# Kernel optimization log

Hardware: AMD Instinct MI355X
Metric: run time of the kernel (lower is better)

## Reference

```python
import jax, jax.numpy as jnp
import numpy as np

D_MODEL = 1024
N_HEADS = 16
HEAD_DIM = D_MODEL // N_HEADS
SPARSITY = 0.5  # torch.rand(...) < sparsity_factor -> True means masked (disallowed)


def setup_inputs() -> dict:
    key = jax.random.key(0)
    ks = jax.random.split(key, 12)
    B, S, D = 2, 2048, D_MODEL
    query = jax.random.normal(ks[0], (B, S, D), dtype=jnp.float32)
    key_t = jax.random.normal(ks[1], (B, S, D), dtype=jnp.float32)
    value = jax.random.normal(ks[2], (B, S, D), dtype=jnp.float32)
    # per-forward random boolean mask, materialized deterministically here
    mask = jax.random.uniform(ks[3], (B, S, S)) < SPARSITY
    scale = 1.0 / np.sqrt(D)
    Wq = jax.random.uniform(ks[4], (D, D), jnp.float32, -scale, scale)
    Wk = jax.random.uniform(ks[5], (D, D), jnp.float32, -scale, scale)
    Wv = jax.random.uniform(ks[6], (D, D), jnp.float32, -scale, scale)
    Wo = jax.random.uniform(ks[7], (D, D), jnp.float32, -scale, scale)
    bq = jnp.zeros((D,), jnp.float32)
    bk = jnp.zeros((D,), jnp.float32)
    bv = jnp.zeros((D,), jnp.float32)
    bo = jnp.zeros((D,), jnp.float32)
    return {"query": query, "key": key_t, "value": value, "mask": mask,
            "Wq": Wq, "Wk": Wk, "Wv": Wv, "Wo": Wo,
            "bq": bq, "bk": bk, "bv": bv, "bo": bo}


def reference(query, key, value, mask, Wq, Wk, Wv, Wo, bq, bk, bv, bo):
    B, S, D = query.shape
    H, hd = N_HEADS, HEAD_DIM
    # in-projections (torch uses x @ W.T + b)
    q = (query @ Wq.T + bq).reshape(B, S, H, hd).transpose(0, 2, 1, 3)  # (B,H,S,hd)
    k = (key @ Wk.T + bk).reshape(B, S, H, hd).transpose(0, 2, 1, 3)
    v = (value @ Wv.T + bv).reshape(B, S, H, hd).transpose(0, 2, 1, 3)
    scores = jnp.einsum('bhqd,bhkd->bhqk', q, k) / jnp.sqrt(jnp.float32(hd))
    # bool mask: True = disallowed; broadcast over heads
    scores = jnp.where(mask[:, None, :, :], -jnp.inf, scores)
    attn = jax.nn.softmax(scores, axis=-1)  # dropout inactive at eval
    out = jnp.einsum('bhqk,bhkd->bhqd', attn, v)  # (B,H,S,hd)
    out = out.transpose(0, 2, 1, 3).reshape(B, S, D)
    return out @ Wo.T + bo
```

## Files before the change

### kernel.cpp

```cpp
#include <hip/hip_runtime.h>
#include <stdint.h>

#define MTOK   4096
#define DMODEL 1024
#define SEQ    2048
#define NH     16
#define HD     64
#define LDK    72
#define LDP    72
#define QSCL   0.18033688f
#define NWORDS (2 * SEQ * SEQ / 64)

typedef _Float16 h8  __attribute__((ext_vector_type(8)));
typedef _Float16 h4  __attribute__((ext_vector_type(4)));
typedef _Float16 h2  __attribute__((ext_vector_type(2)));
typedef __fp16   fp16x2 __attribute__((ext_vector_type(2)));
typedef float    f16v __attribute__((ext_vector_type(16)));
typedef float    f4  __attribute__((ext_vector_type(4)));

typedef __attribute__((address_space(1))) const unsigned int g_u32;
typedef __attribute__((address_space(3))) unsigned int       l_u32;

__device__ __forceinline__ void g2l16(const void* g, void* l) {
    __builtin_amdgcn_global_load_lds((g_u32*)(unsigned long long)g,
                                     (l_u32*)(unsigned int)(unsigned long long)l,
                                     16, 0, 0);
}

__device__ __forceinline__ h2 pkrtz(float a, float b) {
    fp16x2 r = __builtin_amdgcn_cvt_pkrtz(a, b);
    return __builtin_bit_cast(h2, r);
}

#if __has_builtin(__builtin_amdgcn_exp2f)
#define E2(x) __builtin_amdgcn_exp2f(x)
#else
#define E2(x) exp2f(x)
#endif

__global__ __launch_bounds__(256) void prep_kernel(
    const float* __restrict__ s0, const float* __restrict__ s1,
    const float* __restrict__ s2, const float* __restrict__ s3,
    const float* __restrict__ s4, const float* __restrict__ s5,
    const float* __restrict__ s6,
    _Float16* __restrict__ d0, _Float16* __restrict__ d1,
    _Float16* __restrict__ d2, _Float16* __restrict__ d3,
    _Float16* __restrict__ d4, _Float16* __restrict__ d5,
    _Float16* __restrict__ d6,
    const unsigned char* __restrict__ mb, const unsigned int* __restrict__ mu,
    unsigned long long* __restrict__ mout) {
    const int z = blockIdx.y;
    const int gid = blockIdx.x * 256 + threadIdx.x;
    const int stride = gridDim.x * 256;
    if (z < 7) {
        const float* s = (z == 0) ? s0 : (z == 1) ? s1 : (z == 2) ? s2
                       : (z == 3) ? s3 : (z == 4) ? s4 : (z == 5) ? s5 : s6;
        _Float16* d = (z == 0) ? d0 : (z == 1) ? d1 : (z == 2) ? d2
                    : (z == 3) ? d3 : (z == 4) ? d4 : (z == 5) ? d5 : d6;
        const int n4 = (z < 3) ? (MTOK * DMODEL / 4) : (DMODEL * DMODEL / 4);
        for (int i = gid; i < n4; i += stride) {
            float4 v = ((const float4*)s)[i];
            h4 o = {(_Float16)v.x, (_Float16)v.y, (_Float16)v.z, (_Float16)v.w};
            ((h4*)d)[i] = o;
        }
    } else {
        __shared__ int wsum[4];
        int cnt = 0;
        const uchar4* mp4 = (const uchar4*)mb;
#pragma unroll
        for (int i = 0; i < 8; ++i) {
            uchar4 v = mp4[threadIdx.x * 8 + i];
            cnt += (v.x != 0) + (v.y != 0) + (v.z != 0) + (v.w != 0);
        }
#pragma unroll
        for (int off = 32; off > 0; off >>= 1) cnt += __shfl_down(cnt, off, 64);
        if ((threadIdx.x & 63) == 0) wsum[threadIdx.x >> 6] = cnt;
        __syncthreads();
        const int byteflag = (wsum[0] + wsum[1] + wsum[2] + wsum[3]) > 2500;

        for (int w = gid; w < NWORDS; w += stride) {
            unsigned long long bits = 0ull;
            if (byteflag) {
                const uint4* p = (const uint4*)(mb + (size_t)w * 64);
#pragma unroll
                for (int i = 0; i < 4; ++i) {
                    uint4 v = p[i];
                    unsigned dw[4] = {v.x, v.y, v.z, v.w};
#pragma unroll
                    for (int j = 0; j < 4; ++j) {
                        unsigned d = dw[j];
                        unsigned nib = (unsigned)((d & 0xFFu) != 0)
                                     | ((unsigned)((d & 0xFF00u) != 0) << 1)
                                     | ((unsigned)((d & 0xFF0000u) != 0) << 2)
                                     | ((unsigned)((d >> 24) != 0) << 3);
                        bits |= (unsigned long long)nib << (i * 16 + j * 4);
                    }
                }
            } else {
                const uint4* p = (const uint4*)(mu + (size_t)w * 64);
#pragma unroll
                for (int i = 0; i < 16; ++i) {
                    uint4 v = p[i];
                    unsigned nib = (unsigned)(v.x != 0u)
                                 | ((unsigned)(v.y != 0u) << 1)
                                 | ((unsigned)(v.z != 0u) << 2)
                                 | ((unsigned)(v.w != 0u) << 3);
                    bits |= (unsigned long long)nib << (i * 4);
                }
            }
            mout[w] = bits;
        }
    }
}

template <int MODE, int BM, int BN>
__device__ __forceinline__ void gemm16_body(const _Float16* __restrict__ A,
                                            const _Float16* __restrict__ W,
                                            const float* __restrict__ bias,
                                            void* __restrict__ outv,
                                            float scale) {
    __shared__ __align__(16) _Float16 Asb[BM * 64];
    __shared__ __align__(16) _Float16 Bsb[BN * 64];
    constexpr int NI = BM / 32, NJ = BN / 32;
    constexpr int WM = BM / 2,  WN = BN / 2;
    constexpr int RA = BM * 128 / 4096;
    constexpr int RB = BN * 128 / 4096;
    const int tid = threadIdx.x;
    const int wv = tid >> 6, lane = tid & 63;
    const int l15 = lane & 15, g = lane >> 4;
    const int wy = wv >> 1, wx = wv & 1;
    const int m0 = blockIdx.x * BM, n0 = blockIdx.y * BN;

    f4 acc[NI][NJ];
#pragma unroll
    for (int i = 0; i < NI; ++i)
#pragma unroll
        for (int j = 0; j < NJ; ++j) acc[i][j] = (f4){0.f, 0.f, 0.f, 0.f};

    const char* Ab = (const char*)A;
    const char* Wb = (const char*)W;
    int srowA[RA], scolA[RA];
#pragma unroll
    for (int r = 0; r < RA; ++r) {
        const int o = (r * 256 + tid) * 16;
        srowA[r] = o >> 7;
        scolA[r] = (((o >> 4) & 7) ^ (srowA[r] & 7)) * 16;
    }
    int srowB[RB], scolB[RB];
#pragma unroll
    for (int r = 0; r < RB; ++r) {
        const int o = (r * 256 + tid) * 16;
        srowB[r] = o >> 7;
        scolB[r] = (((o >> 4) & 7) ^ (srowB[r] & 7)) * 16;
    }

    for (int kt = 0; kt < 16; ++kt) {
        const int k0b = kt * 128;
        __syncthreads();
#pragma unroll
        for (int r = 0; r < RA; ++r)
            g2l16(Ab + (size_t)(m0 + srowA[r]) * 2048 + k0b + scolA[r],
                  (char*)Asb + (r * 256 + tid) * 16);
#pragma unroll
        for (int r = 0; r < RB; ++r)
            g2l16(Wb + (size_t)(n0 + srowB[r]) * 2048 + k0b + scolB[r],
                  (char*)Bsb + (r * 256 + tid) * 16);
        __syncthreads();

#pragma unroll
        for (int ksub = 0; ksub < 2; ++ksub) {
            h8 af[NI], bf[NJ];
#pragma unroll
            for (int t = 0; t < NI; ++t) {
                const int row = wy * WM + t * 16 + l15;
                const int pos = (ksub * 4 + g) ^ (row & 7);
                af[t] = *(const h8*)(Asb + row * 64 + pos * 8);
            }
#pragma unroll
            for (int t = 0; t < NJ; ++t) {
                const int row = wx * WN + t * 16 + l15;
                const int pos = (ksub * 4 + g) ^ (row & 7);
                bf[t] = *(const h8*)(Bsb + row * 64 + pos * 8);
            }
#pragma unroll
            for (int i = 0; i < NI; ++i)
#pragma unroll
                for (int j = 0; j < NJ; ++j) {
                    if (MODE == 2)
                        acc[i][j] = __builtin_amdgcn_mfma_f32_16x16x32_f16(
                            bf[j], af[i], acc[i][j], 0, 0, 0);
                    else
                        acc[i][j] = __builtin_amdgcn_mfma_f32_16x16x32_f16(
                            af[i], bf[j], acc[i][j], 0, 0, 0);
                }
        }
    }

#pragma unroll
    for (int j = 0; j < NJ; ++j) {
#pragma unroll
        for (int i = 0; i < NI; ++i) {
            if (MODE == 2) {
                const int m = m0 + wy * WM + i * 16 + l15;
                const int b = m >> 11, s = m & 2047;
#pragma unroll
                for (int r = 0; r < 4; ++r) {
                    const int n = n0 + wx * WN + j * 16 + g * 4 + r;
                    const int h = n >> 6, d = n & 63;
                    ((_Float16*)outv)[(((size_t)(b * NH + h)) * HD + d) * SEQ + s] =
                        (_Float16)(acc[i][j][r] + bias[n]);
                }
            } else {
                const int n = n0 + wx * WN + j * 16 + l15;
                const float bb = bias[n];
                const int mbase = m0 + wy * WM + i * 16 + g * 4;
                if (MODE == 1) {
                    const int h = n >> 6, d = n & 63;
#pragma unroll
                    for (int r = 0; r < 4; ++r) {
                        const int m = mbase + r;
                        const int b = m >> 11, s = m & 2047;
                        ((_Float16*)outv)[(((size_t)(b * NH + h)) * SEQ + s) * HD + d] =
                            (_Float16)((acc[i][j][r] + bb) * scale);
                    }
                } else {
#pragma unroll
                    for (int r = 0; r < 4; ++r)
                        ((float*)outv)[(size_t)(mbase + r) * DMODEL + n] =
                            acc[i][j][r] + bb;
                }
            }
        }
    }
}

__global__ __launch_bounds__(256) void qkv_gemm16_kernel(
    const _Float16* __restrict__ xq, const _Float16* __restrict__ xk,
    const _Float16* __restrict__ xv,
    const _Float16* __restrict__ Wq, const _Float16* __restrict__ Wk,
    const _Float16* __restrict__ Wv,
    const float* __restrict__ bq, const float* __restrict__ bk,
    const float* __restrict__ bv,
    _Float16* __restrict__ q_out, _Float16* __restrict__ k_out,
    _Float16* __restrict__ vt_out) {
    const int z = blockIdx.z;
    if (z == 0)      gemm16_body<1, 128, 128>(xq, Wq, bq, (void*)q_out, QSCL);
    else if (z == 1) gemm16_body<1, 128, 128>(xk, Wk, bk, (void*)k_out, 1.0f);
    else             gemm16_body<2, 128, 128>(xv, Wv, bv, (void*)vt_out, 1.0f);
}

__global__ __launch_bounds__(256) void out_gemm16_kernel(
    const _Float16* __restrict__ X, const _Float16* __restrict__ W,
    const float* __restrict__ bias, float* __restrict__ out) {
    gemm16_body<0, 64, 128>(X, W, bias, (void*)out, 1.0f);
}

__global__ __launch_bounds__(256) void attn_kernel(
    const _Float16* __restrict__ Q, const _Float16* __restrict__ K,
    const _Float16* __restrict__ Vt,
    const unsigned long long* __restrict__ mbits,
    _Float16* __restrict__ out) {
    __shared__ __align__(16) _Float16 Ks[2][64 * LDK];
    __shared__ __align__(16) _Float16 Vs[2][64 * LDK];
    __shared__ __align__(16) _Float16 Ps[128 * LDP];

    const int tid = threadIdx.x;
    const int wv = tid >> 6, lane = tid & 63;
    const int l31 = lane & 31, hi = lane >> 5;
    const int q0 = blockIdx.x * 128;
    const int bh = blockIdx.y;
    const int b = bh >> 4, h = bh & 15;
    const size_t bho = (size_t)bh * (SEQ * HD);
    const int qrow = q0 + wv * 32 + l31;

    h8 qf[4];
    const _Float16* qp = Q + bho + (size_t)qrow * HD;
#pragma unroll
    for (int ks = 0; ks < 4; ++ks) qf[ks] = *(const h8*)(qp + ks * 16 + hi * 8);

    f16v Ot[2];
#pragma unroll
    for (int mt = 0; mt < 2; ++mt)
#pragma unroll
        for (int r = 0; r < 16; ++r) Ot[mt][r] = 0.f;
    float l_r = 0.f;

    const int sr = tid >> 2;
    const int scol = (tid & 3) * 16;
    const _Float16* kg = K + bho;
    const _Float16* vg = Vt + bho;
    _Float16* prow = &Ps[(wv * 32 + l31) * LDP];
    const unsigned long long* mrow =
        mbits + ((size_t)b * SEQ + qrow) * (SEQ / 64);

    h8 kr0 = *(const h8*)(kg + (size_t)sr * HD + scol);
    h8 kr1 = *(const h8*)(kg + (size_t)sr * HD + scol + 8);
    h8 vr0 = *(const h8*)(vg + (size_t)sr * SEQ + scol);
    h8 vr1 = *(const h8*)(vg + (size_t)sr * SEQ + scol + 8);
    uint2 mw = *(const uint2*)(mrow);
    *(h8*)(&Ks[0][sr * LDK + scol])     = kr0;
    *(h8*)(&Ks[0][sr * LDK + scol + 8]) = kr1;
    *(h8*)(&Vs[0][sr * LDK + scol])     = vr0;
    *(h8*)(&Vs[0][sr * LDK + scol + 8]) = vr1;
    __syncthreads();

    for (int kt = 0; kt < 32; ++kt) {
        const int cur = kt & 1;
        uint2 mw_n;
        if (kt < 31) {
            const int k0n = (kt + 1) * 64;
            kr0 = *(const h8*)(kg + (size_t)(k0n + sr) * HD + scol);
            kr1 = *(const h8*)(kg + (size_t)(k0n + sr) * HD + scol + 8);
            vr0 = *(const h8*)(vg + (size_t)sr * SEQ + k0n + scol);
            vr1 = *(const h8*)(vg + (size_t)sr * SEQ + k0n + scol + 8);
            mw_n = *(const uint2*)(mrow + kt + 1);
        }

        f16v sc0, sc1;
#pragma unroll
        for (int r = 0; r < 16; ++r) { sc0[r] = 0.f; sc1[r] = 0.f; }
#pragma unroll
        for (int ks = 0; ks < 4; ++ks) {
            h8 kf0 = *(const h8*)(&Ks[cur][l31 * LDK + ks * 16 + hi * 8]);
            h8 kf1 = *(const h8*)(&Ks[cur][(32 + l31) * LDK + ks * 16 + hi * 8]);
            sc0 = __builtin_amdgcn_mfma_f32_32x32x16_f16(kf0, qf[ks], sc0, 0, 0, 0);
            sc1 = __builtin_amdgcn_mfma_f32_32x32x16_f16(kf1, qf[ks], sc1, 0, 0, 0);
        }

        float ps = 0.f;
#pragma unroll
        for (int mt = 0; mt < 2; ++mt) {
            const unsigned w = mt ? mw.y : mw.x;
            const f16v& s = mt ? sc1 : sc0;
#pragma unroll
            for (int g4 = 0; g4 < 4; ++g4) {
                const int sh = g4 * 8 + hi * 4;
                float p0 = E2(((w >> (sh + 0)) & 1u) ? -1e30f : s[g4 * 4 + 0]);
                float p1 = E2(((w >> (sh + 1)) & 1u) ? -1e30f : s[g4 * 4 + 1]);
                float p2 = E2(((w >> (sh + 2)) & 1u) ? -1e30f : s[g4 * 4 + 2]);
                float p3 = E2(((w >> (sh + 3)) & 1u) ? -1e30f : s[g4 * 4 + 3]);
                h2 lo  = pkrtz(p0, p1);
                h2 hi2 = pkrtz(p2, p3);
                ps += p0 + p1 + p2 + p3;
                h4 ph = {lo.x, lo.y, hi2.x, hi2.y};
                *(h4*)(prow + mt * 32 + g4 * 8 + hi * 4) = ph;
            }
        }
        l_r += ps;

        h8 pf[4];
#pragma unroll
        for (int ks = 0; ks < 4; ++ks)
            pf[ks] = *(const h8*)(prow + ks * 16 + hi * 8);
#pragma unroll
        for (int ks = 0; ks < 4; ++ks) {
            h8 vf0 = *(const h8*)(&Vs[cur][l31 * LDK + ks * 16 + hi * 8]);
            h8 vf1 = *(const h8*)(&Vs[cur][(32 + l31) * LDK + ks * 16 + hi * 8]);
            Ot[0] = __builtin_amdgcn_mfma_f32_32x32x16_f16(vf0, pf[ks], Ot[0], 0, 0, 0);
            Ot[1] = __builtin_amdgcn_mfma_f32_32x32x16_f16(vf1, pf[ks], Ot[1], 0, 0, 0);
        }

        if (kt < 31) {
            const int nxt = cur ^ 1;
            *(h8*)(&Ks[nxt][sr * LDK + scol])     = kr0;
            *(h8*)(&Ks[nxt][sr * LDK + scol + 8]) = kr1;
            *(h8*)(&Vs[nxt][sr * LDK + scol])     = vr0;
            *(h8*)(&Vs[nxt][sr * LDK + scol + 8]) = vr1;
            mw = mw_n;
        }
        __syncthreads();
    }

    l_r += __shfl_xor(l_r, 32);
    const float inv = 1.0f / l_r;
    _Float16* op = out + ((size_t)b * SEQ + qrow) * DMODEL + h * HD;
#pragma unroll
    for (int mt = 0; mt < 2; ++mt)
#pragma unroll
        for (int g4 = 0; g4 < 4; ++g4) {
            const int d = mt * 32 + g4 * 8 + hi * 4;
            h4 ov = {(_Float16)(Ot[mt][g4 * 4 + 0] * inv),
                     (_Float16)(Ot[mt][g4 * 4 + 1] * inv),
                     (_Float16)(Ot[mt][g4 * 4 + 2] * inv),
                     (_Float16)(Ot[mt][g4 * 4 + 3] * inv)};
            *(h4*)(op + d) = ov;
        }
}

extern "C" void kernel_launch(void* const* d_in, const int* in_sizes, int n_in,
                              void* d_out, int out_size, void* d_ws, size_t ws_size,
                              hipStream_t stream) {
    const float* query = (const float*)d_in[0];
    const float* key_  = (const float*)d_in[1];
    const float* value = (const float*)d_in[2];
    const void*  mask  = d_in[3];
    const float* Wq = (const float*)d_in[4];
    const float* Wk = (const float*)d_in[5];
    const float* Wv = (const float*)d_in[6];
    const float* Wo = (const float*)d_in[7];
    const float* bq = (const float*)d_in[8];
    const float* bk = (const float*)d_in[9];
    const float* bv = (const float*)d_in[10];
    const float* bo = (const float*)d_in[11];

    char* ws = (char*)d_ws;
    _Float16* xq  = (_Float16*)(ws + 256);
    _Float16* xk  = xq + (size_t)MTOK * DMODEL;
    _Float16* xv  = xk + (size_t)MTOK * DMODEL;
    _Float16* Wqh = xv + (size_t)MTOK * DMODEL;
    _Float16* Wkh = Wqh + (size_t)DMODEL * DMODEL;
    _Float16* Wvh = Wkh + (size_t)DMODEL * DMODEL;
    _Float16* Woh = Wvh + (size_t)DMODEL * DMODEL;
    _Float16* q_ws  = Woh + (size_t)DMODEL * DMODEL;
    _Float16* k_ws  = q_ws + (size_t)MTOK * DMODEL;
    _Float16* vt_ws = k_ws + (size_t)MTOK * DMODEL;
    _Float16* a_ws  = vt_ws + (size_t)MTOK * DMODEL;
    unsigned long long* mb_ws =
        (unsigned long long*)(a_ws + (size_t)MTOK * DMODEL);

    prep_kernel<<<dim3(1024, 8), 256, 0, stream>>>(
        query, key_, value, Wq, Wk, Wv, Wo, xq, xk, xv, Wqh, Wkh, Wvh, Woh,
        (const unsigned char*)mask, (const unsigned int*)mask, mb_ws);

    dim3 gqkv(MTOK / 128, DMODEL / 128, 3);
    qkv_gemm16_kernel<<<gqkv, 256, 0, stream>>>(xq, xk, xv, Wqh, Wkh, Wvh,
                                                bq, bk, bv, q_ws, k_ws, vt_ws);

    dim3 gattn(SEQ / 128, 2 * NH);
    attn_kernel<<<gattn, 256, 0, stream>>>(q_ws, k_ws, vt_ws, mb_ws, a_ws);

    dim3 gout(MTOK / 64, DMODEL / 128);
    out_gemm16_kernel<<<gout, 256, 0, stream>>>(a_ws, Woh, bo, (float*)d_out);
}
```

Baseline: 270.3 us.

## Fuse fp32-to-fp16 activation conversion into QKV GEMM with register prefetch

The separate conversion of query/key/value activations to fp16 in the prep kernel is removed. The QKV GEMM now loads fp32 rows directly into registers, prefetches the next K tile during compute, and converts to fp16 before storing into shared memory. This drops the extra write and re-read of the three fp16 activation copies, but the A-operand path loses the asynchronous global-to-LDS load and each block reads twice as many bytes for A. The attention shared-memory row pitch is also changed from 72 to 76, which affects bank conflicts.

```diff
diff --git a/kernel.cpp b/kernel.cpp
--- a/kernel.cpp
+++ b/kernel.cpp
@@ -6,8 +6,8 @@
 #define SEQ    2048
 #define NH     16
 #define HD     64
-#define LDK    72
-#define LDP    72
+#define LDK    76
+#define LDP    76
 #define QSCL   0.18033688f
 #define NWORDS (2 * SEQ * SEQ / 64)
 
@@ -41,23 +41,17 @@
 __global__ __launch_bounds__(256) void prep_kernel(
     const float* __restrict__ s0, const float* __restrict__ s1,
     const float* __restrict__ s2, const float* __restrict__ s3,
-    const float* __restrict__ s4, const float* __restrict__ s5,
-    const float* __restrict__ s6,
     _Float16* __restrict__ d0, _Float16* __restrict__ d1,
     _Float16* __restrict__ d2, _Float16* __restrict__ d3,
-    _Float16* __restrict__ d4, _Float16* __restrict__ d5,
-    _Float16* __restrict__ d6,
     const unsigned char* __restrict__ mb, const unsigned int* __restrict__ mu,
     unsigned long long* __restrict__ mout) {
     const int z = blockIdx.y;
     const int gid = blockIdx.x * 256 + threadIdx.x;
     const int stride = gridDim.x * 256;
-    if (z < 7) {
-        const float* s = (z == 0) ? s0 : (z == 1) ? s1 : (z == 2) ? s2
-                       : (z == 3) ? s3 : (z == 4) ? s4 : (z == 5) ? s5 : s6;
-        _Float16* d = (z == 0) ? d0 : (z == 1) ? d1 : (z == 2) ? d2
-                    : (z == 3) ? d3 : (z == 4) ? d4 : (z == 5) ? d5 : d6;
-        const int n4 = (z < 3) ? (MTOK * DMODEL / 4) : (DMODEL * DMODEL / 4);
+    if (z < 4) {
+        const float* s = (z == 0) ? s0 : (z == 1) ? s1 : (z == 2) ? s2 : s3;
+        _Float16* d = (z == 0) ? d0 : (z == 1) ? d1 : (z == 2) ? d2 : d3;
+        const int n4 = DMODEL * DMODEL / 4;
         for (int i = gid; i < n4; i += stride) {
             float4 v = ((const float4*)s)[i];
             h4 o = {(_Float16)v.x, (_Float16)v.y, (_Float16)v.z, (_Float16)v.w};
@@ -113,8 +107,8 @@
     }
 }
 
-template <int MODE, int BM, int BN>
-__device__ __forceinline__ void gemm16_body(const _Float16* __restrict__ A,
+template <int MODE, int BM, int BN, int AF32>
+__device__ __forceinline__ void gemm16_body(const void* __restrict__ Ap,
                                             const _Float16* __restrict__ W,
                                             const float* __restrict__ bias,
                                             void* __restrict__ outv,
@@ -137,14 +131,15 @@
 #pragma unroll
         for (int j = 0; j < NJ; ++j) acc[i][j] = (f4){0.f, 0.f, 0.f, 0.f};
 
-    const char* Ab = (const char*)A;
+    const char* Ab = (const char*)Ap;
+    const float* Af = (const float*)Ap;
     const char* Wb = (const char*)W;
     int srowA[RA], scolA[RA];
 #pragma unroll
     for (int r = 0; r < RA; ++r) {
         const int o = (r * 256 + tid) * 16;
         srowA[r] = o >> 7;
-        scolA[r] = (((o >> 4) & 7) ^ (srowA[r] & 7)) * 16;
+        scolA[r] = ((o >> 4) & 7) ^ (srowA[r] & 7);
     }
     int srowB[RB], scolB[RB];
 #pragma unroll
@@ -154,18 +149,50 @@
         scolB[r] = (((o >> 4) & 7) ^ (srowB[r] & 7)) * 16;
     }
 
+    float4 apre[RA][2];
+    if (AF32) {
+#pragma unroll
+        for (int r = 0; r < RA; ++r) {
+            const float* p = Af + (size_t)(m0 + srowA[r]) * 1024 + scolA[r] * 8;
+            apre[r][0] = *(const float4*)(p);
+            apre[r][1] = *(const float4*)(p + 4);
+        }
+    }
+
     for (int kt = 0; kt < 16; ++kt) {
         const int k0b = kt * 128;
         __syncthreads();
-#pragma unroll
-        for (int r = 0; r < RA; ++r)
-            g2l16(Ab + (size_t)(m0 + srowA[r]) * 2048 + k0b + scolA[r],
-                  (char*)Asb + (r * 256 + tid) * 16);
+        if (AF32) {
+#pragma unroll
+            for (int r = 0; r < RA; ++r) {
+                float4 a = apre[r][0], b = apre[r][1];
+                h2 p0 = pkrtz(a.x, a.y), p1 = pkrtz(a.z, a.w);
+                h2 p2 = pkrtz(b.x, b.y), p3 = pkrtz(b.z, b.w);
+                h8 hv = {p0.x, p0.y, p1.x, p1.y, p2.x, p2.y, p3.x, p3.y};
+                *(h8*)((char*)Asb + (r * 256 + tid) * 16) = hv;
+            }
+        } else {
+#pragma unroll
+            for (int r = 0; r < RA; ++r)
+                g2l16(Ab + (size_t)(m0 + srowA[r]) * 2048 + k0b + scolA[r] * 16,
+                      (char*)Asb + (r * 256 + tid) * 16);
+        }
 #pragma unroll
         for (int r = 0; r < RB; ++r)
             g2l16(Wb + (size_t)(n0 + srowB[r]) * 2048 + k0b + scolB[r],
                   (char*)Bsb + (r * 256 + tid) * 16);
         __syncthreads();
+
+        if (AF32 && kt < 15) {
+            const int kf = (kt + 1) * 64;
+#pragma unroll
+            for (int r = 0; r < RA; ++r) {
+                const float* p =
+                    Af + (size_t)(m0 + srowA[r]) * 1024 + kf + scolA[r] * 8;
+                apre[r][0] = *(const float4*)(p);
+                apre[r][1] = *(const float4*)(p + 4);
+            }
+        }
 
 #pragma unroll
         for (int ksub = 0; ksub < 2; ++ksub) {
@@ -235,8 +262,8 @@
 }
 
 __global__ __launch_bounds__(256) void qkv_gemm16_kernel(
-    const _Float16* __restrict__ xq, const _Float16* __restrict__ xk,
-    const _Float16* __restrict__ xv,
+    const float* __restrict__ xq, const float* __restrict__ xk,
+    const float* __restrict__ xv,
     const _Float16* __restrict__ Wq, const _Float16* __restrict__ Wk,
     const _Float16* __restrict__ Wv,
     const float* __restrict__ bq, const float* __restrict__ bk,
@@ -244,15 +271,15 @@
     _Float16* __restrict__ q_out, _Float16* __restrict__ k_out,
     _Float16* __restrict__ vt_out) {
     const int z = blockIdx.z;
-    if (z == 0)      gemm16_body<1, 128, 128>(xq, Wq, bq, (void*)q_out, QSCL);
-    else if (z == 1) gemm16_body<1, 128, 128>(xk, Wk, bk, (void*)k_out, 1.0f);
-    else             gemm16_body<2, 128, 128>(xv, Wv, bv, (void*)vt_out, 1.0f);
+    if (z == 0)      gemm16_body<1, 128, 128, 1>(xq, Wq, bq, (void*)q_out, QSCL);
+    else if (z == 1) gemm16_body<1, 128, 128, 1>(xk, Wk, bk, (void*)k_out, 1.0f);
+    else             gemm16_body<2, 128, 128, 1>(xv, Wv, bv, (void*)vt_out, 1.0f);
 }
 
 __global__ __launch_bounds__(256) void out_gemm16_kernel(
     const _Float16* __restrict__ X, const _Float16* __restrict__ W,
     const float* __restrict__ bias, float* __restrict__ out) {
-    gemm16_body<0, 64, 128>(X, W, bias, (void*)out, 1.0f);
+    gemm16_body<0, 64, 128, 0>(X, W, bias, (void*)out, 1.0f);
 }
 
 __global__ __launch_bounds__(256) void attn_kernel(
@@ -404,10 +431,7 @@
     const float* bo = (const float*)d_in[11];
 
     char* ws = (char*)d_ws;
-    _Float16* xq  = (_Float16*)(ws + 256);
-    _Float16* xk  = xq + (size_t)MTOK * DMODEL;
-    _Float16* xv  = xk + (size_t)MTOK * DMODEL;
-    _Float16* Wqh = xv + (size_t)MTOK * DMODEL;
+    _Float16* Wqh = (_Float16*)(ws + 256);
     _Float16* Wkh = Wqh + (size_t)DMODEL * DMODEL;
     _Float16* Wvh = Wkh + (size_t)DMODEL * DMODEL;
     _Float16* Woh = Wvh + (size_t)DMODEL * DMODEL;
@@ -418,12 +442,13 @@
     unsigned long long* mb_ws =
         (unsigned long long*)(a_ws + (size_t)MTOK * DMODEL);
 
-    prep_kernel<<<dim3(1024, 8), 256, 0, stream>>>(
-        query, key_, value, Wq, Wk, Wv, Wo, xq, xk, xv, Wqh, Wkh, Wvh, Woh,
+    prep_kernel<<<dim3(1024, 5), 256, 0, stream>>>(
+        Wq, Wk, Wv, Wo, Wqh, Wkh, Wvh, Woh,
         (const unsigned char*)mask, (const unsigned int*)mask, mb_ws);
 
     dim3 gqkv(MTOK / 128, DMODEL / 128, 3);
-    qkv_gemm16_kernel<<<gqkv, 256, 0, stream>>>(xq, xk, xv, Wqh, Wkh, Wvh,
+    qkv_gemm16_kernel<<<gqkv, 256, 0, stream>>>(query, key_, value,
+                                                Wqh, Wkh, Wvh,
                                                 bq, bk, bv, q_ws, k_ws, vt_ws);
 
     dim3 gattn(SEQ / 128, 2 * NH);
```

Measured after the change: 324.3 us. 20.0% more time.
